# Kernel optimization log

Measured on AMD Instinct MI355X. Metric: run time of the kernel, lower is better.

The kernel has to match this reference:

```python
import jax, jax.numpy as jnp
import numpy as np

B, N, C = 8, 1024, 768
H = 12
HD = C // H  # 64
SCALE = HD ** -0.5


def setup_inputs() -> dict:
    key = jax.random.key(0)
    k1, k2, k3, k4 = jax.random.split(key, 4)
    x = jax.random.normal(k1, (B, N, C), dtype=jnp.float32)
    # torch Linear weights are [out, in]; qkv has no bias (qkv_bias=False)
    w_qkv = jax.random.normal(k2, (3 * C, C), dtype=jnp.float32) * (C ** -0.5)
    w_proj = jax.random.normal(k3, (C, C), dtype=jnp.float32) * (C ** -0.5)
    b_proj = jax.random.normal(k4, (C,), dtype=jnp.float32) * 0.01
    return {"x": x, "w_qkv": w_qkv, "w_proj": w_proj, "b_proj": b_proj}


def reference(x, w_qkv, w_proj, b_proj):
    b, n, c = x.shape
    # qkv: [B, N, 3C] -> [3, B, H, N, HD]
    qkv = (x @ w_qkv.T).reshape(b, n, 3, H, c // H).transpose(2, 0, 3, 1, 4)
    q, k, v = qkv[0], qkv[1], qkv[2]
    attn = jnp.einsum('bhqd,bhkd->bhqk', q, k) * SCALE
    attn = jax.nn.softmax(attn, axis=-1)
    out = jnp.einsum('bhqk,bhkd->bhqd', attn, v)          # [B, H, N, HD]
    out = out.transpose(0, 2, 1, 3).reshape(b, n, c)      # [B, N, C]
    out = out @ w_proj.T + b_proj
    return out
```

## Files before the change

### kernel.cpp

```cpp
#include <hip/hip_runtime.h>
#include <hip/hip_bf16.h>
#include <cstdint>

#define TB 8
#define TN 1024
#define TC 768
#define TH 12
#define THD 64
#define TM (TB*TN)
#define TNQKV (3*TC)
#define QSCALE_LOG2E 0.18033688011112042f
#define THR_BITS 11.541560327111708f

typedef __attribute__((ext_vector_type(8))) short s16x8;
typedef __attribute__((ext_vector_type(4))) short s16x4;
typedef __attribute__((ext_vector_type(4))) float f32x4;
typedef __attribute__((ext_vector_type(2))) unsigned int u32x2;

__device__ __forceinline__ unsigned short f2bf(float f) {
    union { float f; unsigned int u; } v; v.f = f;
    unsigned int u = v.u;
    return (unsigned short)((u + 0x7FFFu + ((u >> 16) & 1u)) >> 16);
}

__device__ __forceinline__ float bf2f(unsigned short h) {
    union { float f; unsigned int u; } v; v.u = ((unsigned int)h) << 16;
    return v.f;
}

__device__ __forceinline__ unsigned int cvt_pk_bf16(float lo, float hi) {
    unsigned int r;
    asm("v_cvt_pk_bf16_f32 %0, %1, %2" : "=v"(r) : "v"(lo), "v"(hi));
    return r;
}

__device__ __forceinline__ void gload_lds16(const unsigned short* g, unsigned short* l) {
    __builtin_amdgcn_global_load_lds(
        (const __attribute__((address_space(1))) unsigned int*)g,
        (__attribute__((address_space(3))) unsigned int*)l,
        16, 0, 0);
}

__global__ __launch_bounds__(256) void cvt3_kernel(
    const float* __restrict__ a, unsigned short* __restrict__ oa, int na,
    const float* __restrict__ b, unsigned short* __restrict__ ob, int nb,
    const float* __restrict__ c, unsigned short* __restrict__ oc, int nc)
{
    int i = blockIdx.x * blockDim.x + threadIdx.x;
    const float* src; unsigned short* dst; int idx;
    if (i < na)           { src = a; dst = oa; idx = i; }
    else if (i < na + nb) { src = b; dst = ob; idx = i - na; }
    else if (i < na + nb + nc) { src = c; dst = oc; idx = i - na - nb; }
    else return;
    f32x4 x0 = *(const f32x4*)(src + (size_t)idx * 8);
    f32x4 x1 = *(const f32x4*)(src + (size_t)idx * 8 + 4);
    s16x8 r;
    #pragma unroll
    for (int e = 0; e < 4; e++) r[e] = (short)f2bf(x0[e]);
    #pragma unroll
    for (int e = 0; e < 4; e++) r[4 + e] = (short)f2bf(x1[e]);
    *(s16x8*)(dst + (size_t)idx * 8) = r;
}

template<bool BIAS, bool OBF16, bool VSPLIT>
__global__ __launch_bounds__(256) void gemm_bt(
    const unsigned short* __restrict__ A,
    const unsigned short* __restrict__ Bm,
    void* __restrict__ Cout,
    const float* __restrict__ bias,
    unsigned short* __restrict__ vt,
    int M, int Nn, int K)
{
    __shared__ unsigned short As[128 * 64];
    __shared__ unsigned short Bs[128 * 64];
    const int t = threadIdx.x;
    const int w = t >> 6, l = t & 63;
    const int lr = l & 15, lh = l >> 4;
    const int wm = w >> 1, wn = w & 1;
    const int bm = blockIdx.x, bn = blockIdx.y;
    const int lr7 = lr & 7;

    f32x4 acc[4][4] = {};

    const unsigned short* Ab = A + (size_t)bm * 128 * K;
    const unsigned short* Bb = Bm + (size_t)bn * 128 * K;

    for (int kt = 0; kt < K; kt += 64) {
        __syncthreads();
        #pragma unroll
        for (int j = 0; j < 4; j++) {
            const int s = j * 256 + t, row = s >> 3, c = s & 7;
            const int g = c ^ (row & 7);
            gload_lds16(Ab + (size_t)row * K + kt + g * 8, As + s * 8);
            gload_lds16(Bb + (size_t)row * K + kt + g * 8, Bs + s * 8);
        }
        __syncthreads();
        #pragma unroll
        for (int kh = 0; kh < 2; kh++) {
            const int ch = ((kh << 2) + lh) ^ lr7;
            s16x8 af[4], bfr[4];
            #pragma unroll
            for (int mi = 0; mi < 4; mi++)
                af[mi] = *(const s16x8*)(As + (wm * 64 + mi * 16 + lr) * 64 + ch * 8);
            #pragma unroll
            for (int ni = 0; ni < 4; ni++)
                bfr[ni] = *(const s16x8*)(Bs + (wn * 64 + ni * 16 + lr) * 64 + ch * 8);
            #pragma unroll
            for (int mi = 0; mi < 4; mi++)
                #pragma unroll
                for (int ni = 0; ni < 4; ni++)
                    acc[mi][ni] = __builtin_amdgcn_mfma_f32_16x16x32_bf16(
                        af[mi], bfr[ni], acc[mi][ni], 0, 0, 0);
        }
    }

    const int r0 = bm * 128 + wm * 64;
    const int c0 = bn * 128 + wn * 64;
    if constexpr (VSPLIT) {
        if (bn >= 12) {
            #pragma unroll
            for (int mi = 0; mi < 4; mi++) {
                const int row = r0 + mi * 16 + lh * 4;
                const int bb = row >> 10, k = row & 1023;
                #pragma unroll
                for (int ni = 0; ni < 4; ni++) {
                    const int dg = c0 + ni * 16 + lr - 2 * TC;
                    unsigned short* vp = vt + ((size_t)(bb * TH + (dg >> 6)) << 16)
                                            + (dg & 63) * TN + k;
                    u32x2 r;
                    r[0] = cvt_pk_bf16(acc[mi][ni][0], acc[mi][ni][1]);
                    r[1] = cvt_pk_bf16(acc[mi][ni][2], acc[mi][ni][3]);
                    *(u32x2*)vp = r;
                }
            }
            return;
        }
    }
    if constexpr (OBF16) {
        unsigned short* O = (unsigned short*)Cout;
        #pragma unroll
        for (int mi = 0; mi < 4; mi++)
            #pragma unroll
            for (int ni = 0; ni < 4; ni++)
                #pragma unroll
                for (int i = 0; i < 4; i++)
                    O[(size_t)(r0 + mi * 16 + lh * 4 + i) * Nn + c0 + ni * 16 + lr] =
                        f2bf(acc[mi][ni][i]);
    } else {
        float* O = (float*)Cout;
        #pragma unroll
        for (int mi = 0; mi < 4; mi++)
            #pragma unroll
            for (int ni = 0; ni < 4; ni++)
                #pragma unroll
                for (int i = 0; i < 4; i++) {
                    int cc = c0 + ni * 16 + lr;
                    float v = acc[mi][ni][i];
                    if constexpr (BIAS) v += bias[cc];
                    O[(size_t)(r0 + mi * 16 + lh * 4 + i) * Nn + cc] = v;
                }
    }
}

__global__ __launch_bounds__(512) void attn_kernel(
    const unsigned short* __restrict__ qkv,
    const unsigned short* __restrict__ vt,
    unsigned short* __restrict__ out)
{
    const int bid = blockIdx.x;
    const int vid = (bid & 7) * 96 + (bid >> 3);
    const int bh = vid >> 3;
    const int qt = vid & 7;
    const int b = bh / TH, h = bh % TH;
    const int t = threadIdx.x, w = t >> 6, l = t & 63;
    const int lr = l & 15, lh = l >> 4;
    const int qbase = qt * 128 + w * 16;

    __shared__ unsigned short Kbuf[2][64 * 64];
    __shared__ unsigned short Vbuf[2][64 * 64];
    __shared__ unsigned short plds[8][16 * 64];

    const unsigned short* kbase = qkv + (size_t)(b * TN) * TNQKV + TC + h * THD;
    const unsigned short* vtb = vt + (size_t)bh * THD * TN;

    const int srow_lo = (l >> 3);
    const int schunk = (l & 7) ^ srow_lo;
    const int srow = w * 8 + srow_lo;
    const int sdst = w * 512 + l * 8;

    const unsigned short* qptr = qkv + (size_t)(b * TN + qbase + lr) * TNQKV + h * THD;
    s16x8 bq[2];
    #pragma unroll
    for (int cj = 0; cj < 2; cj++) {
        s16x8 raw = *(const s16x8*)(qptr + cj * 32 + lh * 8);
        #pragma unroll
        for (int e = 0; e < 8; e++)
            bq[cj][e] = (short)f2bf(bf2f((unsigned short)raw[e]) * QSCALE_LOG2E);
    }

    f32x4 o[4] = {};
    float m2 = -1e30f, lsum = 0.f;
    unsigned short* pw = plds[w];
    const int lr7 = lr & 7;

    gload_lds16(kbase + (size_t)srow * TNQKV + schunk * 8, &Kbuf[0][sdst]);
    gload_lds16(vtb + (size_t)srow * TN + schunk * 8, &Vbuf[0][sdst]);
    __syncthreads();

    for (int it = 0; it < 16; it++) {
        const int kt = it * 64;
        const int cur = it & 1, nxt = cur ^ 1;
        {
            const int ktn = (kt + 64) & (TN - 1);
            gload_lds16(kbase + (size_t)(ktn + srow) * TNQKV + schunk * 8, &Kbuf[nxt][sdst]);
            gload_lds16(vtb + (size_t)srow * TN + ktn + schunk * 8, &Vbuf[nxt][sdst]);
        }
        const unsigned short* Kc = Kbuf[cur];
        const unsigned short* Vc = Vbuf[cur];

        f32x4 s[4];
        #pragma unroll
        for (int kk = 0; kk < 4; kk++) {
            const int r = kk * 16 + lr;
            s16x8 ak0 = *(const s16x8*)(Kc + r * 64 + ((lh ^ lr7) * 8));
            s16x8 ak1 = *(const s16x8*)(Kc + r * 64 + (((4 + lh) ^ lr7) * 8));
            f32x4 z = {0.f, 0.f, 0.f, 0.f};
            z = __builtin_amdgcn_mfma_f32_16x16x32_bf16(ak0, bq[0], z, 0, 0, 0);
            z = __builtin_amdgcn_mfma_f32_16x16x32_bf16(ak1, bq[1], z, 0, 0, 0);
            s[kk] = z;
        }

        float v[16];
        #pragma unroll
        for (int kk = 0; kk < 4; kk++)
            #pragma unroll
            for (int i = 0; i < 4; i++) v[kk * 4 + i] = s[kk][i];
        float mx = fmaxf(fmaxf(v[0], v[1]), v[2]);
        #pragma unroll
        for (int j = 3; j + 1 < 16; j += 2) mx = fmaxf(fmaxf(mx, v[j]), v[j + 1]);
        mx = fmaxf(mx, v[15]);
        if (!__all(mx <= m2 + THR_BITS)) {
            float rmx = fmaxf(mx, __shfl_xor(mx, 16, 64));
            rmx = fmaxf(rmx, __shfl_xor(rmx, 32, 64));
            float newm = fmaxf(m2, rmx);
            float corr = __builtin_amdgcn_exp2f(m2 - newm);
            m2 = newm;
            lsum *= corr;
            #pragma unroll
            for (int nd = 0; nd < 4; nd++)
                #pragma unroll
                for (int i = 0; i < 4; i++) o[nd][i] *= corr;
        }
        float a[16];
        #pragma unroll
        for (int kk = 0; kk < 4; kk++)
            #pragma unroll
            for (int i = 0; i < 4; i++) {
                float p = __builtin_amdgcn_exp2f(s[kk][i] - m2);
                s[kk][i] = p;
                a[kk * 4 + i] = p;
            }
        #pragma unroll
        for (int st = 8; st >= 1; st >>= 1)
            #pragma unroll
            for (int j = 0; j < st; j++) a[j] += a[j + st];
        lsum += a[0];

        #pragma unroll
        for (int kk = 0; kk < 4; kk++) {
            u32x2 pk;
            pk[0] = cvt_pk_bf16(s[kk][0], s[kk][1]);
            pk[1] = cvt_pk_bf16(s[kk][2], s[kk][3]);
            const int wch = ((kk << 1) + (lh >> 1)) ^ lr7;
            *(u32x2*)(pw + lr * 64 + wch * 8 + (lh & 1) * 4) = pk;
        }
        #pragma unroll
        for (int ktile = 0; ktile < 2; ktile++) {
            const int rch = ((ktile << 2) + lh) ^ lr7;
            s16x8 bp = *(const s16x8*)(pw + lr * 64 + rch * 8);
            #pragma unroll
            for (int nd = 0; nd < 4; nd++) {
                const int d = nd * 16 + lr;
                s16x8 av = *(const s16x8*)(
                    Vc + d * 64 + ((((ktile << 2) + lh) ^ lr7) * 8));
                o[nd] = __builtin_amdgcn_mfma_f32_16x16x32_bf16(av, bp, o[nd], 0, 0, 0);
            }
        }
        __syncthreads();
    }

    lsum += __shfl_xor(lsum, 16, 64);
    lsum += __shfl_xor(lsum, 32, 64);
    float inv = 1.f / lsum;
    unsigned short* op = out + (size_t)(b * TN + qbase + lr) * TC + h * THD;
    #pragma unroll
    for (int nd = 0; nd < 4; nd++) {
        u32x2 r;
        r[0] = cvt_pk_bf16(o[nd][0] * inv, o[nd][1] * inv);
        r[1] = cvt_pk_bf16(o[nd][2] * inv, o[nd][3] * inv);
        *(u32x2*)(op + nd * 16 + lh * 4) = r;
    }
}

extern "C" void kernel_launch(void* const* d_in, const int* in_sizes, int n_in,
                              void* d_out, int out_size, void* d_ws, size_t ws_size,
                              hipStream_t stream) {
    const float* x      = (const float*)d_in[0];
    const float* w_qkv  = (const float*)d_in[1];
    const float* w_proj = (const float*)d_in[2];
    const float* b_proj = (const float*)d_in[3];
    float* out = (float*)d_out;

    unsigned short* xb   = (unsigned short*)d_ws;
    unsigned short* wqb  = xb   + (size_t)TM * TC;
    unsigned short* wpb  = wqb  + (size_t)TNQKV * TC;
    unsigned short* qkvb = wpb  + (size_t)TC * TC;
    unsigned short* vtb  = qkvb + (size_t)TM * TNQKV;
    unsigned short* aob  = vtb  + (size_t)TB * TH * THD * TN;

    const int na = TM * TC / 8, nb = TNQKV * TC / 8, nc = TC * TC / 8;
    cvt3_kernel<<<(na + nb + nc + 255) / 256, 256, 0, stream>>>(
        x, xb, na, w_qkv, wqb, nb, w_proj, wpb, nc);

    gemm_bt<false, true, true><<<dim3(TM / 128, TNQKV / 128), 256, 0, stream>>>(
        xb, wqb, (void*)qkvb, nullptr, vtb, TM, TNQKV, TC);

    attn_kernel<<<768, 512, 0, stream>>>(qkvb, vtb, aob);

    gemm_bt<true, false, false><<<dim3(TM / 128, TC / 128), 256, 0, stream>>>(
        aob, wpb, (void*)out, b_proj, nullptr, TM, TC, TC);
}
```

Measured before the change: 123.8 us.

## Use 32x32x16 MFMA in GEMMs and compute softmax row sums via MFMA

The projection GEMM kernel moves from a 4x4 grid of 16x16x32 MFMA tiles per wave to a 2x2 grid of 32x32x16 MFMA tiles, with matching LDS fragment loads and epilogue index mapping. This cuts LDS fragment reads and instruction count per K step. In the attention kernel, the per-tile softmax denominator is no longer a scalar reduction plus cross-lane shuffles. Instead an extra MFMA multiplies the bf16 probabilities by a ones vector, which folds the row sum into the matrix pipe. The sum now comes from bf16-rounded probabilities, a small numerical change, and it costs one extra MFMA per k-subtile.

```diff
diff --git a/kernel.cpp b/kernel.cpp
--- a/kernel.cpp
+++ b/kernel.cpp
@@ -15,6 +15,7 @@
 typedef __attribute__((ext_vector_type(8))) short s16x8;
 typedef __attribute__((ext_vector_type(4))) short s16x4;
 typedef __attribute__((ext_vector_type(4))) float f32x4;
+typedef __attribute__((ext_vector_type(16))) float f32x16;
 typedef __attribute__((ext_vector_type(2))) unsigned int u32x2;
 
 __device__ __forceinline__ unsigned short f2bf(float f) {
@@ -75,12 +76,13 @@
     __shared__ unsigned short Bs[128 * 64];
     const int t = threadIdx.x;
     const int w = t >> 6, l = t & 63;
-    const int lr = l & 15, lh = l >> 4;
+    const int lh = l >> 4;
     const int wm = w >> 1, wn = w & 1;
     const int bm = blockIdx.x, bn = blockIdx.y;
-    const int lr7 = lr & 7;
-
-    f32x4 acc[4][4] = {};
+    const int l31 = l & 31, khi = l >> 5;
+    const int r7 = l31 & 7;
+
+    f32x16 acc00 = {}, acc01 = {}, acc10 = {}, acc11 = {};
 
     const unsigned short* Ab = A + (size_t)bm * 128 * K;
     const unsigned short* Bb = Bm + (size_t)bn * 128 * K;
@@ -96,69 +98,74 @@
         }
         __syncthreads();
         #pragma unroll
-        for (int kh = 0; kh < 2; kh++) {
-            const int ch = ((kh << 2) + lh) ^ lr7;
-            s16x8 af[4], bfr[4];
-            #pragma unroll
-            for (int mi = 0; mi < 4; mi++)
-                af[mi] = *(const s16x8*)(As + (wm * 64 + mi * 16 + lr) * 64 + ch * 8);
-            #pragma unroll
-            for (int ni = 0; ni < 4; ni++)
-                bfr[ni] = *(const s16x8*)(Bs + (wn * 64 + ni * 16 + lr) * 64 + ch * 8);
-            #pragma unroll
-            for (int mi = 0; mi < 4; mi++)
-                #pragma unroll
-                for (int ni = 0; ni < 4; ni++)
-                    acc[mi][ni] = __builtin_amdgcn_mfma_f32_16x16x32_bf16(
-                        af[mi], bfr[ni], acc[mi][ni], 0, 0, 0);
+        for (int ks = 0; ks < 4; ks++) {
+            const int ch = ((ks << 1) + khi) ^ r7;
+            const unsigned short* Ar = As + (wm * 64 + l31) * 64 + ch * 8;
+            const unsigned short* Br = Bs + (wn * 64 + l31) * 64 + ch * 8;
+            s16x8 a0 = *(const s16x8*)(Ar);
+            s16x8 a1 = *(const s16x8*)(Ar + 32 * 64);
+            s16x8 b0 = *(const s16x8*)(Br);
+            s16x8 b1 = *(const s16x8*)(Br + 32 * 64);
+            acc00 = __builtin_amdgcn_mfma_f32_32x32x16_bf16(a0, b0, acc00, 0, 0, 0);
+            acc01 = __builtin_amdgcn_mfma_f32_32x32x16_bf16(a0, b1, acc01, 0, 0, 0);
+            acc10 = __builtin_amdgcn_mfma_f32_32x32x16_bf16(a1, b0, acc10, 0, 0, 0);
+            acc11 = __builtin_amdgcn_mfma_f32_32x32x16_bf16(a1, b1, acc11, 0, 0, 0);
         }
     }
 
     const int r0 = bm * 128 + wm * 64;
     const int c0 = bn * 128 + wn * 64;
+    f32x16 accs[2][2] = {{acc00, acc01}, {acc10, acc11}};
     if constexpr (VSPLIT) {
         if (bn >= 12) {
-            #pragma unroll
-            for (int mi = 0; mi < 4; mi++) {
-                const int row = r0 + mi * 16 + lh * 4;
-                const int bb = row >> 10, k = row & 1023;
+            const int bb = (r0 >> 10) * TH;
+            #pragma unroll
+            for (int X = 0; X < 2; X++)
                 #pragma unroll
-                for (int ni = 0; ni < 4; ni++) {
-                    const int dg = c0 + ni * 16 + lr - 2 * TC;
-                    unsigned short* vp = vt + ((size_t)(bb * TH + (dg >> 6)) << 16)
-                                            + (dg & 63) * TN + k;
-                    u32x2 r;
-                    r[0] = cvt_pk_bf16(acc[mi][ni][0], acc[mi][ni][1]);
-                    r[1] = cvt_pk_bf16(acc[mi][ni][2], acc[mi][ni][3]);
-                    *(u32x2*)vp = r;
+                for (int Y = 0; Y < 2; Y++) {
+                    const int dg = c0 + Y * 32 + l31 - 2 * TC;
+                    unsigned short* vp = vt + ((size_t)(bb + (dg >> 6)) << 16)
+                                            + (dg & 63) * TN;
+                    const int k0 = (r0 & 1023) + X * 32 + 4 * khi;
+                    #pragma unroll
+                    for (int g = 0; g < 4; g++) {
+                        u32x2 r;
+                        r[0] = cvt_pk_bf16(accs[X][Y][g * 4], accs[X][Y][g * 4 + 1]);
+                        r[1] = cvt_pk_bf16(accs[X][Y][g * 4 + 2], accs[X][Y][g * 4 + 3]);
+                        *(u32x2*)(vp + k0 + 8 * g) = r;
+                    }
                 }
-            }
             return;
         }
     }
     if constexpr (OBF16) {
         unsigned short* O = (unsigned short*)Cout;
         #pragma unroll
-        for (int mi = 0; mi < 4; mi++)
-            #pragma unroll
-            for (int ni = 0; ni < 4; ni++)
+        for (int X = 0; X < 2; X++)
+            #pragma unroll
+            for (int Y = 0; Y < 2; Y++) {
+                const int cc = c0 + Y * 32 + l31;
+                const int rb = r0 + X * 32 + 4 * khi;
                 #pragma unroll
-                for (int i = 0; i < 4; i++)
-                    O[(size_t)(r0 + mi * 16 + lh * 4 + i) * Nn + c0 + ni * 16 + lr] =
-                        f2bf(acc[mi][ni][i]);
+                for (int i = 0; i < 16; i++)
+                    O[(size_t)(rb + (i & 3) + 8 * (i >> 2)) * Nn + cc] =
+                        f2bf(accs[X][Y][i]);
+            }
     } else {
         float* O = (float*)Cout;
         #pragma unroll
-        for (int mi = 0; mi < 4; mi++)
-            #pragma unroll
-            for (int ni = 0; ni < 4; ni++)
+        for (int X = 0; X < 2; X++)
+            #pragma unroll
+            for (int Y = 0; Y < 2; Y++) {
+                const int cc = c0 + Y * 32 + l31;
+                const int rb = r0 + X * 32 + 4 * khi;
+                float bv = 0.f;
+                if constexpr (BIAS) bv = bias[cc];
                 #pragma unroll
-                for (int i = 0; i < 4; i++) {
-                    int cc = c0 + ni * 16 + lr;
-                    float v = acc[mi][ni][i];
-                    if constexpr (BIAS) v += bias[cc];
-                    O[(size_t)(r0 + mi * 16 + lh * 4 + i) * Nn + cc] = v;
-                }
+                for (int i = 0; i < 16; i++)
+                    O[(size_t)(rb + (i & 3) + 8 * (i >> 2)) * Nn + cc] =
+                        accs[X][Y][i] + bv;
+            }
     }
 }
 
@@ -197,9 +204,12 @@
         for (int e = 0; e < 8; e++)
             bq[cj][e] = (short)f2bf(bf2f((unsigned short)raw[e]) * QSCALE_LOG2E);
     }
-
-    f32x4 o[4] = {};
-    float m2 = -1e30f, lsum = 0.f;
+    s16x8 av1;
+    #pragma unroll
+    for (int e = 0; e < 8; e++) av1[e] = (short)0x3F80;
+
+    f32x4 o[5] = {};
+    float m2 = -1e30f;
     unsigned short* pw = plds[w];
     const int lr7 = lr & 7;
 
@@ -245,26 +255,16 @@
             float newm = fmaxf(m2, rmx);
             float corr = __builtin_amdgcn_exp2f(m2 - newm);
             m2 = newm;
-            lsum *= corr;
-            #pragma unroll
-            for (int nd = 0; nd < 4; nd++)
+            #pragma unroll
+            for (int nd = 0; nd < 5; nd++)
                 #pragma unroll
                 for (int i = 0; i < 4; i++) o[nd][i] *= corr;
         }
-        float a[16];
         #pragma unroll
         for (int kk = 0; kk < 4; kk++)
             #pragma unroll
-            for (int i = 0; i < 4; i++) {
-                float p = __builtin_amdgcn_exp2f(s[kk][i] - m2);
-                s[kk][i] = p;
-                a[kk * 4 + i] = p;
-            }
-        #pragma unroll
-        for (int st = 8; st >= 1; st >>= 1)
-            #pragma unroll
-            for (int j = 0; j < st; j++) a[j] += a[j + st];
-        lsum += a[0];
+            for (int i = 0; i < 4; i++)
+                s[kk][i] = __builtin_amdgcn_exp2f(s[kk][i] - m2);
 
         #pragma unroll
         for (int kk = 0; kk < 4; kk++) {
@@ -285,13 +285,12 @@
                     Vc + d * 64 + ((((ktile << 2) + lh) ^ lr7) * 8));
                 o[nd] = __builtin_amdgcn_mfma_f32_16x16x32_bf16(av, bp, o[nd], 0, 0, 0);
             }
+            o[4] = __builtin_amdgcn_mfma_f32_16x16x32_bf16(av1, bp, o[4], 0, 0, 0);
         }
         __syncthreads();
     }
 
-    lsum += __shfl_xor(lsum, 16, 64);
-    lsum += __shfl_xor(lsum, 32, 64);
-    float inv = 1.f / lsum;
+    float inv = 1.f / o[4][0];
     unsigned short* op = out + (size_t)(b * TN + qbase + lr) * TC + h * THD;
     #pragma unroll
     for (int nd = 0; nd < 4; nd++) {
```

Measured after the change: 113.4 us. -8.4%, faster.
